# Performance work log

Measured on AMD Instinct MI355X. Metric: run time of the kernel, lower is better.

The kernel has to match this reference:

```python
import jax, jax.numpy as jnp
import numpy as np

EPS_BN = 1e-5
EPS_SIM = 1e-8
PAD = 1
NUM_ITERS = 3


def capsule_conv2d(x, w):
    # x: [B, C, H, W]; w: [out_caps, in_caps, kh, kw, in_len, out_len]
    B, C, H, W = x.shape
    oc, ic, kh, kw, il, ol = w.shape
    # im2col patches, feature dim ordered (c, kh, kw) -> matches torch.unfold
    patches = jax.lax.conv_general_dilated_patches(
        x, (kh, kw), (1, 1), [(PAD, PAD), (PAD, PAD)])  # [B, C*kh*kw, H, W]
    N = H * W
    p = patches.reshape(B, ic, il, kh * kw, N)
    p = jnp.transpose(p, (0, 4, 1, 3, 2))  # [B, N, ic, kk, il]
    wf = w.reshape(oc, ic, kh * kw, il, ol)
    # per-patch capsule transform -> priors [B, N, oc, ic*kk, ol]
    priors = jnp.einsum('bnikl,oiklm->bnoikm', p, wf)
    priors = priors.reshape(B, N, oc, ic * kh * kw, ol)
    # k-means routing with Tonimoto similarity, 3 iterations, no squash
    out = priors.mean(axis=-2, keepdims=True)  # [B, N, oc, 1, ol]
    for _ in range(NUM_ITERS):
        dot = jnp.sum(priors * out, axis=-1, keepdims=True)
        n1 = jnp.sum(priors * priors, axis=-1, keepdims=True)
        n2 = jnp.sum(out * out, axis=-1, keepdims=True)
        logits = dot / jnp.maximum(n1 + n2 - dot, EPS_SIM)
        probs = jax.nn.softmax(logits, axis=-2)
        out = jnp.sum(probs * priors, axis=-2, keepdims=True)
    out = out[..., 0, :]                      # [B, N, oc, ol]
    out = out.reshape(B, H, W, oc * ol)       # channels = oc*ol
    return jnp.transpose(out, (0, 3, 1, 2))   # [B, C, H, W]


def batchnorm2d(x, gamma, beta):
    mean = x.mean(axis=(0, 2, 3), keepdims=True)
    var = x.var(axis=(0, 2, 3), keepdims=True)  # biased, as torch BN training fwd
    inv = jax.lax.rsqrt(var + EPS_BN)
    return gamma[None, :, None, None] * (x - mean) * inv + beta[None, :, None, None]


def setup_inputs() -> dict:
    key = jax.random.key(0)
    k0, k1, k2 = jax.random.split(key, 3)
    B, C, H, W = 2, 64, 96, 96
    IL = OL = 8
    x = jax.random.normal(k0, (B, C, H, W), jnp.float32)
    w1 = jax.random.normal(k1, (C // OL, C // IL, 3, 3, IL, OL), jnp.float32) * 0.1
    w2 = jax.random.normal(k2, (C // OL, C // OL, 3, 3, OL, OL), jnp.float32) * 0.1
    g1 = jnp.ones((C,), jnp.float32)
    b1 = jnp.zeros((C,), jnp.float32)
    g2 = jnp.ones((C,), jnp.float32)
    b2 = jnp.zeros((C,), jnp.float32)
    return {"x": x, "w1": w1, "g1": g1, "b1": b1, "w2": w2, "g2": g2, "b2": b2}


def reference(x, w1, g1, b1, w2, g2, b2):
    r = batchnorm2d(capsule_conv2d(x, w1), g1, b1)
    r = batchnorm2d(capsule_conv2d(r, w2), g2, b2)
    return x + r
```

## Files before the change

### kernel.cpp

```cpp
#include <hip/hip_runtime.h>
#include <hip/hip_bf16.h>

#define HW 9216
#define NPC 18432
#define NELEM 1179648
#define XSTR 72
#define PATCH_B 7776
#define XREC 12
#define XBUF_B (4*2*16*2*XREC*4)

typedef __attribute__((ext_vector_type(2))) float f32x2;
typedef __attribute__((ext_vector_type(4))) float f32x4v;
typedef __attribute__((ext_vector_type(8))) short short8v;

__device__ __forceinline__ int detect_is32(const unsigned short* __restrict__ w1u) {
    int lane = threadIdx.x & 63;
    int bad = 0;
    #pragma unroll
    for (int i = 0; i < 16; ++i) {
        unsigned short u = (unsigned short)(w1u[lane + i * 64] & 0x7FFF);
        bad |= (u >= 0x42C8);
    }
    return (__ballot(bad) != 0ULL) ? 1 : 0;
}

__device__ __forceinline__ float load_in(const void* p, int idx, int is32) {
    return is32 ? ((const float*)p)[idx]
                : __bfloat162float(((const __hip_bfloat16*)p)[idx]);
}

__device__ __forceinline__ float lo16(unsigned v) { return __int_as_float((int)(v << 16)); }
__device__ __forceinline__ float hi16(unsigned v) { return __int_as_float((int)(v & 0xFFFF0000u)); }
__device__ __forceinline__ float bfu(unsigned short u) { return __int_as_float((int)u << 16); }
__device__ __forceinline__ unsigned pk2bf(float a, float b) {
    __hip_bfloat162 h = __float22bfloat162_rn(float2{a, b});
    return *(unsigned*)&h;
}

__device__ __forceinline__ float dotsq4(const f32x4v a) {
    float t = a[0] * a[0];
    t = fmaf(a[1], a[1], t);
    t = fmaf(a[2], a[2], t);
    t = fmaf(a[3], a[3], t);
    return t;
}
__device__ __forceinline__ float dot4(const f32x4v a, const float om[4]) {
    float t = a[0] * om[0];
    t = fmaf(a[1], om[1], t);
    t = fmaf(a[2], om[2], t);
    t = fmaf(a[3], om[3], t);
    return t;
}

__launch_bounds__(256)
__global__ void prep_kernel(const void* __restrict__ x,
                            const void* __restrict__ w1, const void* __restrict__ w2,
                            __hip_bfloat16* __restrict__ xt,
                            __hip_bfloat16* __restrict__ Bfr1,
                            __hip_bfloat16* __restrict__ Bfr2,
                            float* __restrict__ statz) {
    __shared__ float tile[64 * 33];
    const int bid = blockIdx.x;
    if (bid < 576) {
        const int is32 = detect_is32((const unsigned short*)w1);
        int xb = bid % 3, y = (bid / 3) % 96, b = bid / 288;
        int x0 = xb * 32;
        for (int e = threadIdx.x; e < 512; e += 256) {
            int xl4 = (e & 7) * 4, c = e >> 3;
            int base = ((b * 64 + c) * 96 + y) * 96 + x0 + xl4;
            float4 v;
            if (is32) {
                v = *(const float4*)&((const float*)x)[base];
            } else {
                ushort4 u = *(const ushort4*)&((const unsigned short*)x)[base];
                v = make_float4(bfu(u.x), bfu(u.y), bfu(u.z), bfu(u.w));
            }
            tile[c * 33 + xl4 + 0] = v.x;
            tile[c * 33 + xl4 + 1] = v.y;
            tile[c * 33 + xl4 + 2] = v.z;
            tile[c * 33 + xl4 + 3] = v.w;
        }
        __syncthreads();
        for (int f = threadIdx.x; f < 512; f += 256) {
            int c4 = f & 15, xl = f >> 4;
            float a0 = tile[(4 * c4 + 0) * 33 + xl];
            float a1 = tile[(4 * c4 + 1) * 33 + xl];
            float a2 = tile[(4 * c4 + 2) * 33 + xl];
            float a3 = tile[(4 * c4 + 3) * 33 + xl];
            uint2 w;
            w.x = pk2bf(a0, a1);
            w.y = pk2bf(a2, a3);
            *(uint2*)&xt[((b * 96 + y) * 96 + x0 + xl) * 64 + c4 * 4] = w;
        }
    } else if (bid < 720) {
        const int is32 = detect_is32((const unsigned short*)w1);
        int t = (bid - 576) * 256 + threadIdx.x;
        int layer = t / 18432;
        int r = t - layer * 18432;
        int lane = r & 63;
        int fi = r >> 6;
        int h = fi & 1, g = (fi >> 1) & 1;
        int kq = fi >> 2;
        int k = kq % 9, o = kq / 9;
        int dy = k / 3, dx = k % 3;
        int quad = lane >> 4, colhi = (lane >> 3) & 1, m = lane & 7;
        int heff = h ^ (m >> 2);
        int act = (quad == 2 * heff + colhi);
        int i = g * 4 + 2 * heff + colhi;
        const void* w = layer ? w2 : w1;
        __hip_bfloat16* dst = layer ? Bfr2 : Bfr1;
        #pragma unroll
        for (int j = 0; j < 8; ++j) {
            float v = act ? load_in(w, ((((o * 8 + i) * 3 + dy) * 3 + dx) * 8 + j) * 8 + m, is32)
                          : 0.f;
            dst[(fi * 64 + lane) * 8 + j] = __float2bfloat16(v);
        }
    } else {
        for (int e = threadIdx.x; e < 2048; e += 256) statz[e] = 0.f;
    }
}

__device__ __forceinline__ void xexchange(float* __restrict__ xbufF, int slot,
                                          int o2w, int pos16, int g, int quad,
                                          int mhalf, float ac[4], float& se) {
    float* rec = xbufF + ((((slot * 2 + o2w) * 16 + pos16) * 2 + g) * XREC);
    if (quad < 2) {
        *(float4*)(rec + quad * 4) = make_float4(ac[0], ac[1], ac[2], ac[3]);
        if (quad == 0) rec[8] = se;
    }
    __syncthreads();
    const float* prec = xbufF + ((((slot * 2 + o2w) * 16 + pos16) * 2 + (1 - g)) * XREC);
    float4 po = *(const float4*)(prec + mhalf * 4);
    ac[0] += po.x; ac[1] += po.y; ac[2] += po.z; ac[3] += po.w;
    se += prec[8];
}

__launch_bounds__(256, 4)
__global__ void caps_kernel(const __hip_bfloat16* __restrict__ in,
                            const float* __restrict__ statPrev,
                            const void* __restrict__ gamma, const void* __restrict__ beta,
                            const void* __restrict__ wdt,
                            const __hip_bfloat16* __restrict__ Bfr,
                            __hip_bfloat16* __restrict__ yout,
                            float* __restrict__ statL,
                            int layer1) {
    __shared__ __align__(16) unsigned char smem[PATCH_B + XBUF_B];
    __hip_bfloat16* patchH = (__hip_bfloat16*)smem;
    float* xbufF = (float*)(smem + PATCH_B);
    float* omF = (float*)smem;
    float* scL = (float*)(smem + PATCH_B);
    float* shL = scL + 64;

    const int gx    = blockIdx.x;
    const int opair = gx & 3;
    const int x0    = (gx >> 2) * 16;
    const int y  = blockIdx.y;
    const int b  = blockIdx.z;
    const int tid = threadIdx.x;

    if (!layer1) {
        if (tid < 64) {
            const int is32 = detect_is32((const unsigned short*)wdt);
            int c = tid;
            float s = 0.f, ss = 0.f;
            #pragma unroll
            for (int cp = 0; cp < 8; ++cp) {
                s  += statPrev[cp * 128 + c];
                ss += statPrev[cp * 128 + 64 + c];
            }
            float mean = s * (1.f / (float)NPC);
            float var  = fmaxf(ss * (1.f / (float)NPC) - mean * mean, 0.f);
            float inv  = rsqrtf(var + 1e-5f);
            float g = load_in(gamma, c, is32) * inv;
            scL[c] = g;
            shL[c] = load_in(beta, c, is32) - mean * g;
        }
        __syncthreads();
    }

    for (int e = tid; e < 864; e += 256) {
        int c4 = e & 15;
        int q  = e >> 4;
        int xo = q % 18, row = q / 18;
        int yy = y + row - 1, xx = x0 + xo - 1;
        uint2 v = {0u, 0u};
        if (yy >= 0 && yy < 96 && xx >= 0 && xx < 96) {
            v = *(const uint2*)&in[((b * 96 + yy) * 96 + xx) * 64 + c4 * 4];
            if (!layer1) {
                int c = c4 * 4;
                float f0 = lo16(v.x) * scL[c]     + shL[c];
                float f1 = hi16(v.x) * scL[c + 1] + shL[c + 1];
                float f2 = lo16(v.y) * scL[c + 2] + shL[c + 2];
                float f3 = hi16(v.y) * scL[c + 3] + shL[c + 3];
                v.x = pk2bf(f0, f1);
                v.y = pk2bf(f2, f3);
            }
        }
        *(uint2*)&patchH[q * XSTR + c4 * 4] = v;
    }
    __syncthreads();

    const int lane  = tid & 63;
    const int wv    = tid >> 6;
    const int o2w   = wv >> 1;
    const int g     = wv & 1;
    const int pos16 = lane & 15;
    const int quad  = lane >> 4;
    const int mhalf = quad & 1;

    f32x4v P[9][2];
    {
        const int o = opair * 2 + o2w;
        #pragma unroll
        for (int k = 0; k < 9; ++k) {
            const int dy = k / 3, dx = k % 3;
            short8v a = *(const short8v*)&patchH[(dy * 18 + dx + pos16) * XSTR + g * 32 + quad * 8];
            #pragma unroll
            for (int h = 0; h < 2; ++h) {
                short8v bf = *(const short8v*)&Bfr[((((o * 9 + k) * 2 + g) * 2 + h) * 64 + lane) * 8];
                P[k][h] = __builtin_amdgcn_mfma_f32_16x16x32_bf16(bf, a, (f32x4v){0.f, 0.f, 0.f, 0.f}, 0, 0, 0);
            }
        }
    }
    #pragma unroll
    for (int k = 0; k < 9; ++k) {
        asm("" : "+v"(P[k][0]));
        asm("" : "+v"(P[k][1]));
    }

    float n1o[9];
    #pragma unroll
    for (int k = 0; k < 9; ++k) {
        float np1 = dotsq4(P[k][1]);
        n1o[k] = dotsq4(P[k][0]) + __shfl_xor(np1, 16, 64);
    }

    float om[4];
    {
        float ac[4];
        #pragma unroll
        for (int r = 0; r < 4; ++r) {
            float s = 0.f;
            #pragma unroll
            for (int k = 0; k < 9; ++k) s += P[k][0][r] + P[k][1][r];
            s += __shfl_xor(s, 32, 64);
            ac[r] = s;
        }
        float dummy = 0.f;
        xexchange(xbufF, 0, o2w, pos16, g, quad, mhalf, ac, dummy);
        #pragma unroll
        for (int r = 0; r < 4; ++r) om[r] = ac[r] * (1.f / 72.f);
    }
    float n2;
    {
        float n2p = dotsq4((f32x4v){om[0], om[1], om[2], om[3]});
        n2 = n2p + __shfl_xor(n2p, 16, 64);
    }

    #pragma unroll
    for (int it = 0; it < 3; ++it) {
        float se = 0.f;
        float ac[4] = {0.f, 0.f, 0.f, 0.f};
        #pragma unroll
        for (int k = 0; k < 9; ++k) {
            float dp0 = dot4(P[k][0], om);
            float dp1 = dot4(P[k][1], om);
            float d = dp0 + __shfl_xor(dp1, 16, 64);
            float denom = fmaxf(n1o[k] + n2 - d, 1e-8f);
            float e = __expf(d * __builtin_amdgcn_rcpf(denom));
            se += e;
            float eo = __shfl_xor(e, 16, 64);
            ac[0] = fmaf(e, P[k][0][0], fmaf(eo, P[k][1][0], ac[0]));
            ac[1] = fmaf(e, P[k][0][1], fmaf(eo, P[k][1][1], ac[1]));
            ac[2] = fmaf(e, P[k][0][2], fmaf(eo, P[k][1][2], ac[2]));
            ac[3] = fmaf(e, P[k][0][3], fmaf(eo, P[k][1][3], ac[3]));
        }
        se += __shfl_xor(se, 16, 64);
        se += __shfl_xor(se, 32, 64);
        #pragma unroll
        for (int r = 0; r < 4; ++r) ac[r] += __shfl_xor(ac[r], 32, 64);
        xexchange(xbufF, 1 + it, o2w, pos16, g, quad, mhalf, ac, se);
        float inv = __builtin_amdgcn_rcpf(se);
        #pragma unroll
        for (int r = 0; r < 4; ++r) om[r] = ac[r] * inv;
        float n2p = dotsq4((f32x4v){om[0], om[1], om[2], om[3]});
        n2 = n2p + __shfl_xor(n2p, 16, 64);
    }

    if (g == 0 && quad < 2) {
        const int o = opair * 2 + o2w;
        uint2 pk;
        pk.x = pk2bf(om[0], om[1]);
        pk.y = pk2bf(om[2], om[3]);
        *(uint2*)&yout[((b * 96 + y) * 96 + x0 + pos16) * 64 + o * 8 + mhalf * 4] = pk;
        *(float4*)&omF[(o2w * 16 + pos16) * 8 + mhalf * 4] = make_float4(om[0], om[1], om[2], om[3]);
    }
    __syncthreads();

    if (tid < 32) {
        int c16 = tid & 15, sel = tid >> 4;
        int oo2 = c16 >> 3, m = c16 & 7;
        float v = 0.f;
        #pragma unroll
        for (int pp = 0; pp < 16; ++pp) {
            float t = omF[(oo2 * 16 + pp) * 8 + m];
            v += sel ? t * t : t;
        }
        int cp = (blockIdx.x + blockIdx.y * 3 + blockIdx.z) & 7;
        atomicAdd(&statL[cp * 128 + sel * 64 + (opair * 2 + oo2) * 8 + m], v);
    }
}

__launch_bounds__(256)
__global__ void final_kernel(const void* __restrict__ xin,
                             const __hip_bfloat16* __restrict__ yt2,
                             const float* __restrict__ statL,
                             const void* __restrict__ gamma, const void* __restrict__ beta,
                             const void* __restrict__ w1,
                             void* __restrict__ outp) {
    __shared__ float tile[64 * 33];
    __shared__ float scL[64], shL[64];
    const int is32 = detect_is32((const unsigned short*)w1);
    if (threadIdx.x < 64) {
        int c = threadIdx.x;
        float s = 0.f, ss = 0.f;
        #pragma unroll
        for (int cp = 0; cp < 8; ++cp) {
            s  += statL[cp * 128 + c];
            ss += statL[cp * 128 + 64 + c];
        }
        float mean = s * (1.f / (float)NPC);
        float var  = fmaxf(ss * (1.f / (float)NPC) - mean * mean, 0.f);
        float inv  = rsqrtf(var + 1e-5f);
        float g = load_in(gamma, c, is32) * inv;
        scL[c] = g;
        shL[c] = load_in(beta, c, is32) - mean * g;
    }
    __syncthreads();

    int x0 = blockIdx.x * 32, y = blockIdx.y, b = blockIdx.z;
    for (int e = threadIdx.x; e < 512; e += 256) {
        int c4 = e & 15, xl = e >> 4;
        uint2 v = *(const uint2*)&yt2[((b * 96 + y) * 96 + x0 + xl) * 64 + c4 * 4];
        int c = c4 * 4;
        tile[(c + 0) * 33 + xl] = lo16(v.x) * scL[c]     + shL[c];
        tile[(c + 1) * 33 + xl] = hi16(v.x) * scL[c + 1] + shL[c + 1];
        tile[(c + 2) * 33 + xl] = lo16(v.y) * scL[c + 2] + shL[c + 2];
        tile[(c + 3) * 33 + xl] = hi16(v.y) * scL[c + 3] + shL[c + 3];
    }
    __syncthreads();
    for (int f = threadIdx.x; f < 512; f += 256) {
        int xl4 = (f & 7) * 4, c = f >> 3;
        int idx = ((b * 64 + c) * 96 + y) * 96 + x0 + xl4;
        float4 xv;
        if (is32) {
            xv = *(const float4*)&((const float*)xin)[idx];
        } else {
            ushort4 u = *(const ushort4*)&((const unsigned short*)xin)[idx];
            xv = make_float4(bfu(u.x), bfu(u.y), bfu(u.z), bfu(u.w));
        }
        float r0 = xv.x + tile[c * 33 + xl4 + 0];
        float r1 = xv.y + tile[c * 33 + xl4 + 1];
        float r2 = xv.z + tile[c * 33 + xl4 + 2];
        float r3 = xv.w + tile[c * 33 + xl4 + 3];
        if (is32) {
            *(float4*)&((float*)outp)[idx] = make_float4(r0, r1, r2, r3);
        } else {
            uint2 w;
            w.x = pk2bf(r0, r1);
            w.y = pk2bf(r2, r3);
            *(uint2*)&((__hip_bfloat16*)outp)[idx] = w;
        }
    }
}

extern "C" void kernel_launch(void* const* d_in, const int* in_sizes, int n_in,
                              void* d_out, int out_size, void* d_ws, size_t ws_size,
                              hipStream_t stream) {
    const void* x  = d_in[0];
    const void* w1 = d_in[1];
    const void* g1 = d_in[2];
    const void* b1 = d_in[3];
    const void* w2 = d_in[4];
    const void* g2 = d_in[5];
    const void* b2 = d_in[6];

    __hip_bfloat16* bufA = (__hip_bfloat16*)d_ws;
    __hip_bfloat16* bufB = bufA + NELEM;
    __hip_bfloat16* Bfr1 = bufB + NELEM;
    __hip_bfloat16* Bfr2 = Bfr1 + 147456;
    float* statz = (float*)(Bfr2 + 147456);
    float* statL1 = statz;
    float* statL2 = statz + 1024;

    prep_kernel<<<721, 256, 0, stream>>>(x, w1, w2, bufA, Bfr1, Bfr2, statz);

    dim3 cgrid(24, 96, 2);
    caps_kernel<<<cgrid, 256, 0, stream>>>(bufA, nullptr, nullptr, nullptr, w1,
                                           Bfr1, bufB, statL1, 1);
    caps_kernel<<<cgrid, 256, 0, stream>>>(bufB, statL1, g1, b1, w1,
                                           Bfr2, bufA, statL2, 0);
    final_kernel<<<dim3(3, 96, 2), 256, 0, stream>>>(x, bufA, statL2, g2, b2, w1, d_out);
}
```

Baseline: 160.1 us.

## Restructure capsule kernel to single-wave blocks with shuffle-only routing reductions

Each capsule block is now one 64-lane wave handling one output capsule over 8 pixels, instead of four waves that exchanged partial routing sums through shared memory with block barriers. The two input-capsule halves are packed into the MFMA's 16 columns (8 pixels each, zero-padded operands) and accumulated by chaining two MFMAs, so all routing reductions become cross-lane shuffles. BN statistics are also reduced by shuffles before the atomics. This removes the __syncthreads exchanges, but it doubles MFMA work through zero padding, re-reads the halo patch for every capsule (8x more blocks), and drops the barrier after the shared-memory patch fill, relying on the block being a single wave.

New measurement: 239.4 us. 49.6% more time.

```diff
diff --git a/kernel.cpp b/kernel.cpp
--- a/kernel.cpp
+++ b/kernel.cpp
@@ -4,10 +4,8 @@
 #define HW 9216
 #define NPC 18432
 #define NELEM 1179648
-#define XSTR 72
-#define PATCH_B 7776
-#define XREC 12
-#define XBUF_B (4*2*16*2*XREC*4)
+#define PSTRIDE 80
+#define ZOFF (30*PSTRIDE)
 
 typedef __attribute__((ext_vector_type(2))) float f32x2;
 typedef __attribute__((ext_vector_type(4))) float f32x4v;
@@ -120,22 +118,7 @@
     }
 }
 
-__device__ __forceinline__ void xexchange(float* __restrict__ xbufF, int slot,
-                                          int o2w, int pos16, int g, int quad,
-                                          int mhalf, float ac[4], float& se) {
-    float* rec = xbufF + ((((slot * 2 + o2w) * 16 + pos16) * 2 + g) * XREC);
-    if (quad < 2) {
-        *(float4*)(rec + quad * 4) = make_float4(ac[0], ac[1], ac[2], ac[3]);
-        if (quad == 0) rec[8] = se;
-    }
-    __syncthreads();
-    const float* prec = xbufF + ((((slot * 2 + o2w) * 16 + pos16) * 2 + (1 - g)) * XREC);
-    float4 po = *(const float4*)(prec + mhalf * 4);
-    ac[0] += po.x; ac[1] += po.y; ac[2] += po.z; ac[3] += po.w;
-    se += prec[8];
-}
-
-__launch_bounds__(256, 4)
+__launch_bounds__(64, 3)
 __global__ void caps_kernel(const __hip_bfloat16* __restrict__ in,
                             const float* __restrict__ statPrev,
                             const void* __restrict__ gamma, const void* __restrict__ beta,
@@ -144,44 +127,38 @@
                             __hip_bfloat16* __restrict__ yout,
                             float* __restrict__ statL,
                             int layer1) {
-    __shared__ __align__(16) unsigned char smem[PATCH_B + XBUF_B];
-    __hip_bfloat16* patchH = (__hip_bfloat16*)smem;
-    float* xbufF = (float*)(smem + PATCH_B);
-    float* omF = (float*)smem;
-    float* scL = (float*)(smem + PATCH_B);
-    float* shL = scL + 64;
-
-    const int gx    = blockIdx.x;
-    const int opair = gx & 3;
-    const int x0    = (gx >> 2) * 16;
+    __shared__ __align__(16) __hip_bfloat16 patchH[30 * PSTRIDE + 8];
+    __shared__ float scL[64], shL[64];
+
+    const int gx = blockIdx.x;
+    const int o  = gx & 7;
+    const int x0 = (gx >> 3) * 8;
     const int y  = blockIdx.y;
     const int b  = blockIdx.z;
-    const int tid = threadIdx.x;
+    const int lane = threadIdx.x;
 
     if (!layer1) {
-        if (tid < 64) {
-            const int is32 = detect_is32((const unsigned short*)wdt);
-            int c = tid;
-            float s = 0.f, ss = 0.f;
-            #pragma unroll
-            for (int cp = 0; cp < 8; ++cp) {
-                s  += statPrev[cp * 128 + c];
-                ss += statPrev[cp * 128 + 64 + c];
-            }
-            float mean = s * (1.f / (float)NPC);
-            float var  = fmaxf(ss * (1.f / (float)NPC) - mean * mean, 0.f);
-            float inv  = rsqrtf(var + 1e-5f);
-            float g = load_in(gamma, c, is32) * inv;
-            scL[c] = g;
-            shL[c] = load_in(beta, c, is32) - mean * g;
-        }
-        __syncthreads();
-    }
-
-    for (int e = tid; e < 864; e += 256) {
+        const int is32 = detect_is32((const unsigned short*)wdt);
+        int c = lane;
+        float s = 0.f, ss = 0.f;
+        #pragma unroll
+        for (int cp = 0; cp < 8; ++cp) {
+            s  += statPrev[cp * 128 + c];
+            ss += statPrev[cp * 128 + 64 + c];
+        }
+        float mean = s * (1.f / (float)NPC);
+        float var  = fmaxf(ss * (1.f / (float)NPC) - mean * mean, 0.f);
+        float inv  = rsqrtf(var + 1e-5f);
+        float g = load_in(gamma, c, is32) * inv;
+        scL[c] = g;
+        shL[c] = load_in(beta, c, is32) - mean * g;
+    }
+    if (lane == 0) *(uint4*)&patchH[ZOFF] = (uint4){0u, 0u, 0u, 0u};
+
+    for (int e = lane; e < 480; e += 64) {
         int c4 = e & 15;
         int q  = e >> 4;
-        int xo = q % 18, row = q / 18;
+        int xo = q % 10, row = q / 10;
         int yy = y + row - 1, xx = x0 + xo - 1;
         uint2 v = {0u, 0u};
         if (yy >= 0 && yy < 96 && xx >= 0 && xx < 96) {
@@ -196,29 +173,32 @@
                 v.y = pk2bf(f2, f3);
             }
         }
-        *(uint2*)&patchH[q * XSTR + c4 * 4] = v;
-    }
-    __syncthreads();
-
-    const int lane  = tid & 63;
-    const int wv    = tid >> 6;
-    const int o2w   = wv >> 1;
-    const int g     = wv & 1;
-    const int pos16 = lane & 15;
-    const int quad  = lane >> 4;
+        *(uint2*)&patchH[q * PSTRIDE + c4 * 4] = v;
+    }
+
+    const int col  = lane & 15;
+    const int quad = lane >> 4;
+    const int isB  = col >> 3;
     const int mhalf = quad & 1;
 
     f32x4v P[9][2];
     {
-        const int o = opair * 2 + o2w;
+        const int pbaseA = col * PSTRIDE + quad * 8;
+        const int pbaseB = (col - 8) * PSTRIDE + 32 + quad * 8;
         #pragma unroll
         for (int k = 0; k < 9; ++k) {
             const int dy = k / 3, dx = k % 3;
-            short8v a = *(const short8v*)&patchH[(dy * 18 + dx + pos16) * XSTR + g * 32 + quad * 8];
+            const int koff = (dy * 10 + dx) * PSTRIDE;
+            const __hip_bfloat16* aApt = &patchH[isB ? ZOFF : (koff + pbaseA)];
+            const __hip_bfloat16* aBpt = &patchH[isB ? (koff + pbaseB) : ZOFF];
+            short8v aA = *(const short8v*)aApt;
+            short8v aB = *(const short8v*)aBpt;
             #pragma unroll
             for (int h = 0; h < 2; ++h) {
-                short8v bf = *(const short8v*)&Bfr[((((o * 9 + k) * 2 + g) * 2 + h) * 64 + lane) * 8];
-                P[k][h] = __builtin_amdgcn_mfma_f32_16x16x32_bf16(bf, a, (f32x4v){0.f, 0.f, 0.f, 0.f}, 0, 0, 0);
+                short8v w0 = *(const short8v*)&Bfr[((((o * 9 + k) * 2 + 0) * 2 + h) * 64 + lane) * 8];
+                short8v w1 = *(const short8v*)&Bfr[((((o * 9 + k) * 2 + 1) * 2 + h) * 64 + lane) * 8];
+                f32x4v t = __builtin_amdgcn_mfma_f32_16x16x32_bf16(w0, aA, (f32x4v){0.f, 0.f, 0.f, 0.f}, 0, 0, 0);
+                P[k][h] = __builtin_amdgcn_mfma_f32_16x16x32_bf16(w1, aB, t, 0, 0, 0);
             }
         }
     }
@@ -236,20 +216,14 @@
     }
 
     float om[4];
-    {
-        float ac[4];
-        #pragma unroll
-        for (int r = 0; r < 4; ++r) {
-            float s = 0.f;
-            #pragma unroll
-            for (int k = 0; k < 9; ++k) s += P[k][0][r] + P[k][1][r];
-            s += __shfl_xor(s, 32, 64);
-            ac[r] = s;
-        }
-        float dummy = 0.f;
-        xexchange(xbufF, 0, o2w, pos16, g, quad, mhalf, ac, dummy);
-        #pragma unroll
-        for (int r = 0; r < 4; ++r) om[r] = ac[r] * (1.f / 72.f);
+    #pragma unroll
+    for (int r = 0; r < 4; ++r) {
+        float s = 0.f;
+        #pragma unroll
+        for (int k = 0; k < 9; ++k) s += P[k][0][r] + P[k][1][r];
+        s += __shfl_xor(s, 32, 64);
+        s += __shfl_xor(s, 8, 64);
+        om[r] = s * (1.f / 72.f);
     }
     float n2;
     {
@@ -277,9 +251,12 @@
         }
         se += __shfl_xor(se, 16, 64);
         se += __shfl_xor(se, 32, 64);
-        #pragma unroll
-        for (int r = 0; r < 4; ++r) ac[r] += __shfl_xor(ac[r], 32, 64);
-        xexchange(xbufF, 1 + it, o2w, pos16, g, quad, mhalf, ac, se);
+        se += __shfl_xor(se, 8, 64);
+        #pragma unroll
+        for (int r = 0; r < 4; ++r) {
+            ac[r] += __shfl_xor(ac[r], 32, 64);
+            ac[r] += __shfl_xor(ac[r], 8, 64);
+        }
         float inv = __builtin_amdgcn_rcpf(se);
         #pragma unroll
         for (int r = 0; r < 4; ++r) om[r] = ac[r] * inv;
@@ -287,27 +264,32 @@
         n2 = n2p + __shfl_xor(n2p, 16, 64);
     }
 
-    if (g == 0 && quad < 2) {
-        const int o = opair * 2 + o2w;
+    if (quad < 2 && col < 8) {
         uint2 pk;
         pk.x = pk2bf(om[0], om[1]);
         pk.y = pk2bf(om[2], om[3]);
-        *(uint2*)&yout[((b * 96 + y) * 96 + x0 + pos16) * 64 + o * 8 + mhalf * 4] = pk;
-        *(float4*)&omF[(o2w * 16 + pos16) * 8 + mhalf * 4] = make_float4(om[0], om[1], om[2], om[3]);
-    }
-    __syncthreads();
-
-    if (tid < 32) {
-        int c16 = tid & 15, sel = tid >> 4;
-        int oo2 = c16 >> 3, m = c16 & 7;
-        float v = 0.f;
-        #pragma unroll
-        for (int pp = 0; pp < 16; ++pp) {
-            float t = omF[(oo2 * 16 + pp) * 8 + m];
-            v += sel ? t * t : t;
-        }
-        int cp = (blockIdx.x + blockIdx.y * 3 + blockIdx.z) & 7;
-        atomicAdd(&statL[cp * 128 + sel * 64 + (opair * 2 + oo2) * 8 + m], v);
+        *(uint2*)&yout[((b * 96 + y) * 96 + x0 + col) * 64 + o * 8 + mhalf * 4] = pk;
+    }
+
+    {
+        float s1[4], sq[4];
+        #pragma unroll
+        for (int r = 0; r < 4; ++r) {
+            float t = om[r];
+            float u = om[r] * om[r];
+            t += __shfl_xor(t, 1, 64);  u += __shfl_xor(u, 1, 64);
+            t += __shfl_xor(t, 2, 64);  u += __shfl_xor(u, 2, 64);
+            t += __shfl_xor(t, 4, 64);  u += __shfl_xor(u, 4, 64);
+            s1[r] = t; sq[r] = u;
+        }
+        if (quad < 2 && col == 0) {
+            int cp = (blockIdx.x + blockIdx.y * 3 + blockIdx.z) & 7;
+            #pragma unroll
+            for (int r = 0; r < 4; ++r) {
+                atomicAdd(&statL[cp * 128 +      o * 8 + mhalf * 4 + r], s1[r]);
+                atomicAdd(&statL[cp * 128 + 64 + o * 8 + mhalf * 4 + r], sq[r]);
+            }
+        }
     }
 }
 
@@ -395,10 +377,10 @@
 
     prep_kernel<<<721, 256, 0, stream>>>(x, w1, w2, bufA, Bfr1, Bfr2, statz);
 
-    dim3 cgrid(24, 96, 2);
-    caps_kernel<<<cgrid, 256, 0, stream>>>(bufA, nullptr, nullptr, nullptr, w1,
-                                           Bfr1, bufB, statL1, 1);
-    caps_kernel<<<cgrid, 256, 0, stream>>>(bufB, statL1, g1, b1, w1,
-                                           Bfr2, bufA, statL2, 0);
+    dim3 cgrid(96, 96, 2);
+    caps_kernel<<<cgrid, 64, 0, stream>>>(bufA, nullptr, nullptr, nullptr, w1,
+                                          Bfr1, bufB, statL1, 1);
+    caps_kernel<<<cgrid, 64, 0, stream>>>(bufB, statL1, g1, b1, w1,
+                                          Bfr2, bufA, statL2, 0);
     final_kernel<<<dim3(3, 96, 2), 256, 0, stream>>>(x, bufA, statL2, g2, b2, w1, d_out);
 }
```
